# Kernel tuning notes

Hardware: AMD Instinct MI355X
Metric: run time of the kernel (lower is better)

Reference implementation:

```python
import jax, jax.numpy as jnp
import numpy as np

FP4_MAX = 6.0
FP8_MAX = 448.0  # float8_e4m3fn max
BLOCK = 16
# representable |values| of fp4 e2m1 and decision midpoints (ties round up)
FP4_LEVELS = jnp.array([0.0, 0.5, 1.0, 1.5, 2.0, 3.0, 4.0, 6.0], dtype=jnp.float32)
FP4_MIDS = jnp.array([0.25, 0.75, 1.25, 1.75, 2.5, 3.5, 5.0], dtype=jnp.float32)


def _fp4_round(x):
    # round to nearest fp4 e2m1 value (magnitudes clamp at 6)
    a = jnp.abs(x)
    idx = jnp.searchsorted(FP4_MIDS, a, side='right')
    return jnp.sign(x) * FP4_LEVELS[idx]


def nvfp4_quant(x, global_scale):
    # x: [M, K] float32 -> (q_fp4 values [M, K], block scales [M, K//16] fp8-representable)
    M, K = x.shape
    xb = x.reshape(M, K // BLOCK, BLOCK)
    block_amax = jnp.max(jnp.abs(xb), axis=-1)  # [M, K//16]
    scale = jnp.clip(block_amax * (global_scale / FP4_MAX), 0.0, FP8_MAX)
    scale = scale.astype(jnp.float8_e4m3fn).astype(jnp.float32)
    safe = jnp.where(scale == 0.0, 1.0, scale)
    q = _fp4_round(xb * (global_scale / safe)[..., None])
    return q.reshape(M, K), scale


def setup_inputs() -> dict:
    key = jax.random.key(0)
    k_in, k_w, k_b = jax.random.split(key, 3)
    M, K, N = 256, 5120, 13824
    x = jax.random.normal(k_in, (M, K), dtype=jnp.float32)
    # build pre-quantized NVFP4 weight buffers (as the module's load_quantized_weights would)
    w = jax.random.normal(k_w, (N, K), dtype=jnp.float32) * 0.02
    w_gs = (FP8_MAX * FP4_MAX) / jnp.max(jnp.abs(w))  # scalar float32
    w_fp4, w_scale = nvfp4_quant(w, w_gs)
    bias = jax.random.normal(k_b, (N,), dtype=jnp.float32) * 0.01
    return {
        'input': x,
        'weight_fp4': w_fp4,            # [N, K] fp4 values held in f32
        'weight_scale': w_scale,        # [N, K//16] fp8_e4m3-representable f32
        'weight_global_scale': w_gs,    # scalar f32
        'bias': bias,                   # [N]
    }


def reference(input, weight_fp4, weight_scale, weight_global_scale, bias):
    # activations cast to bf16 (as in the torch module), math in f32
    x = input.astype(jnp.bfloat16).astype(jnp.float32)
    M, K = x.shape
    N = weight_fp4.shape[0]
    # per-tensor global scale for activations
    a_gs = (FP8_MAX * FP4_MAX) / jnp.max(jnp.abs(x))
    alpha = 1.0 / (a_gs * weight_global_scale)
    # on-the-fly fp4 quantization of activations
    a_fp4, a_scale = nvfp4_quant(x, a_gs)
    # block-scaled dequant-matmul: out = (a_fp4*s_a) @ (w_fp4*s_w)^T * alpha + bias
    a_u = (a_fp4.reshape(M, K // BLOCK, BLOCK) * a_scale[..., None]).reshape(M, K)
    w_u = (weight_fp4.reshape(N, K // BLOCK, BLOCK) * weight_scale[..., None]).reshape(N, K)
    out = jnp.einsum('mk,nk->mn', a_u, w_u) * alpha + bias[None, :]
    return out
```

## Files before the change

kernel.cpp:

```cpp
#include <hip/hip_runtime.h>

typedef __attribute__((ext_vector_type(8))) __bf16 bf16x8;
typedef __attribute__((ext_vector_type(4))) float floatx4;

#define M_TOT 256
#define K_TOT 5120
#define N_TOT 13824
#define NBLK  320
#define BN    64
#define BK    64
#define KSPLIT 4
#define KCH   1280
#define NSTEP 20

#define GLOAD_LDS16(g, l)                                                     \
  __builtin_amdgcn_global_load_lds(                                           \
      (const __attribute__((address_space(1))) void*)(g),                     \
      (__attribute__((address_space(3))) void*)(l), 16, 0, 0)

static __device__ __forceinline__ float bf16r(float v) { return (float)(__bf16)v; }

static __device__ __forceinline__ float fp4round(float v) {
  float a = fabsf(v), q;
  if      (a < 0.25f) q = 0.0f;
  else if (a < 0.75f) q = 0.5f;
  else if (a < 1.25f) q = 1.0f;
  else if (a < 1.75f) q = 1.5f;
  else if (a < 2.5f)  q = 2.0f;
  else if (a < 3.5f)  q = 3.0f;
  else if (a < 5.0f)  q = 4.0f;
  else                q = 6.0f;
  return copysignf(q, v);
}

static __device__ __forceinline__ float cvt_e4m3(float f) {
  if (f < 0.015625f) return rintf(f * 512.0f) * 0.001953125f;
  int e = (int)(__float_as_uint(f) >> 23) - 127;
  float q = __uint_as_float((unsigned)(e - 3 + 127) << 23);
  return rintf(f / q) * q;
}

__global__ void k_amax(const float* __restrict__ x, unsigned* __restrict__ amax_bits) {
  int i = blockIdx.x * blockDim.x + threadIdx.x;
  float4 v = ((const float4*)x)[i];
  float m = fmaxf(fmaxf(fabsf(bf16r(v.x)), fabsf(bf16r(v.y))),
                  fmaxf(fabsf(bf16r(v.z)), fabsf(bf16r(v.w))));
#pragma unroll
  for (int off = 32; off; off >>= 1) m = fmaxf(m, __shfl_xor(m, off));
  if ((threadIdx.x & 63) == 0) atomicMax(amax_bits, __float_as_uint(m));
}

__global__ void k_aquant(const float* __restrict__ x,
                         const unsigned* __restrict__ amax_bits,
                         __bf16* __restrict__ au) {
  int idx = blockIdx.x * blockDim.x + threadIdx.x;
  int m = idx / NBLK;
  int b = idx - m * NBLK;
  float amax = __uint_as_float(*amax_bits);
  float gs  = 2688.0f / amax;
  float gs6 = gs / 6.0f;
  const float4* xp = (const float4*)(x + m * K_TOT + b * 16);
  float4 v0 = xp[0], v1 = xp[1], v2 = xp[2], v3 = xp[3];
  float xv[16];
  xv[0]=bf16r(v0.x); xv[1]=bf16r(v0.y); xv[2]=bf16r(v0.z); xv[3]=bf16r(v0.w);
  xv[4]=bf16r(v1.x); xv[5]=bf16r(v1.y); xv[6]=bf16r(v1.z); xv[7]=bf16r(v1.w);
  xv[8]=bf16r(v2.x); xv[9]=bf16r(v2.y); xv[10]=bf16r(v2.z); xv[11]=bf16r(v2.w);
  xv[12]=bf16r(v3.x); xv[13]=bf16r(v3.y); xv[14]=bf16r(v3.z); xv[15]=bf16r(v3.w);
  float am = 0.f;
#pragma unroll
  for (int j = 0; j < 16; ++j) am = fmaxf(am, fabsf(xv[j]));
  float s = cvt_e4m3(fminf(am * gs6, 448.0f));
  float g = gs / ((s == 0.f) ? 1.f : s);
  bf16x8 p0, p1;
#pragma unroll
  for (int j = 0; j < 8; ++j) p0[j] = (__bf16)(fp4round(xv[j] * g) * s);
#pragma unroll
  for (int j = 0; j < 8; ++j) p1[j] = (__bf16)(fp4round(xv[8 + j] * g) * s);
  bf16x8* dst = (bf16x8*)(au + (size_t)idx * 16);
  dst[0] = p0; dst[1] = p1;
}

__global__ __launch_bounds__(512, 4) void k_gemm(
    const __bf16* __restrict__ au,
    const float*  __restrict__ w,
    const float*  __restrict__ wsc,
    const unsigned* __restrict__ amax_bits,
    const float*  __restrict__ wgs,
    const float*  __restrict__ bias,
    float* __restrict__ out)
{
  __shared__ __bf16 Ab[2][M_TOT * BK];
  __shared__ __bf16 Bb[2][BN * BK];

  const int tid  = threadIdx.x;
  const int lane = tid & 63;
  const int wv   = tid >> 6;
  const int wm   = wv >> 1;
  const int wn   = wv & 1;

  const int s     = blockIdx.x & (KSPLIT - 1);
  const int n0    = (blockIdx.x >> 2) * BN;
  const int kbase = s * KCH;

  const int arow  = wv * 32 + (lane >> 3);
  const int acolp = 8 * ((lane & 7) ^ (lane >> 3));

  const int brow = tid >> 3;
  const int bcg  = tid & 7;
  const float* wp  = w   + (size_t)(n0 + brow) * K_TOT + kbase + bcg * 8;
  const float* wsp = wsc + (size_t)(n0 + brow) * NBLK + s * (KCH / 16) + (bcg >> 1);
  const int bdst = brow * 128 + ((bcg * 16) ^ ((brow & 7) << 4));

  const int sw    = (lane & 7) << 4;
  const int hi    = lane >> 4;
  const int r15   = lane & 15;

  floatx4 acc[4][2];
#pragma unroll
  for (int fm = 0; fm < 4; ++fm)
#pragma unroll
    for (int fn = 0; fn < 2; ++fn) acc[fm][fn] = (floatx4){0.f, 0.f, 0.f, 0.f};

  float4 bv0, bv1; float bs;

  auto issueA = [&](int t, int buf) {
    const __bf16* src = au + (size_t)arow * K_TOT + kbase + t * BK + acolp;
    char* dst = (char*)(&Ab[buf][0]) + wv * 4096;
#pragma unroll
    for (int i = 0; i < 4; ++i)
      GLOAD_LDS16(src + (size_t)i * 8 * K_TOT, dst + i * 1024);
  };
  auto loadB = [&](int t) {
    const float* p = wp + t * BK;
    bv0 = *(const float4*)p;
    bv1 = *(const float4*)(p + 4);
    bs  = wsp[t * 4];
  };
  auto writeB = [&](int buf) {
    float vv[8] = {bv0.x, bv0.y, bv0.z, bv0.w, bv1.x, bv1.y, bv1.z, bv1.w};
    bf16x8 pk;
#pragma unroll
    for (int j = 0; j < 8; ++j) pk[j] = (__bf16)(vv[j] * bs);
    *(bf16x8*)((char*)(&Bb[buf][0]) + bdst) = pk;
  };
  auto compute = [&](int buf) {
    char* pA = (char*)(&Ab[buf][0]);
    char* pB = (char*)(&Bb[buf][0]);
#pragma unroll
    for (int ss = 0; ss < 2; ++ss) {
      const int cb = ss * 64 + hi * 16;
      bf16x8 af[4], bfr[2];
#pragma unroll
      for (int fm = 0; fm < 4; ++fm)
        af[fm] = *(const bf16x8*)(pA + (wm * 64 + fm * 16 + r15) * 128 + (cb ^ sw));
#pragma unroll
      for (int fn = 0; fn < 2; ++fn)
        bfr[fn] = *(const bf16x8*)(pB + (wn * 32 + fn * 16 + r15) * 128 + (cb ^ sw));
#pragma unroll
      for (int fm = 0; fm < 4; ++fm)
#pragma unroll
        for (int fn = 0; fn < 2; ++fn)
          acc[fm][fn] = __builtin_amdgcn_mfma_f32_16x16x32_bf16(af[fm], bfr[fn], acc[fm][fn], 0, 0, 0);
    }
  };

  int buf = 0;
  issueA(0, 0);
  loadB(0);
  writeB(0);
  __syncthreads();
#pragma unroll 1
  for (int t = 0; t < NSTEP; ++t) {
    if (t + 1 < NSTEP) { issueA(t + 1, buf ^ 1); loadB(t + 1); }
    compute(buf);
    if (t + 1 < NSTEP) writeB(buf ^ 1);
    __syncthreads();
    buf ^= 1;
  }

  float amax = __uint_as_float(*amax_bits);
  float a_gs = 2688.0f / amax;
  float alpha = 1.0f / (a_gs * wgs[0]);
#pragma unroll
  for (int fm = 0; fm < 4; ++fm) {
#pragma unroll
    for (int fn = 0; fn < 2; ++fn) {
      int mrow = wm * 64 + fm * 16 + hi * 4;
      int ncol = n0 + wn * 32 + fn * 16 + r15;
      float bb = (s == 0) ? bias[ncol] : 0.0f;
#pragma unroll
      for (int j = 0; j < 4; ++j)
        atomicAdd(&out[(size_t)(mrow + j) * N_TOT + ncol],
                  acc[fm][fn][j] * alpha + bb);
    }
  }
}

extern "C" void kernel_launch(void* const* d_in, const int* in_sizes, int n_in,
                              void* d_out, int out_size, void* d_ws, size_t ws_size,
                              hipStream_t stream) {
  const float* x    = (const float*)d_in[0];
  const float* wq   = (const float*)d_in[1];
  const float* wsc  = (const float*)d_in[2];
  const float* wgs  = (const float*)d_in[3];
  const float* bias = (const float*)d_in[4];
  float* out = (float*)d_out;

  unsigned* amax = (unsigned*)d_ws;
  __bf16* au = (__bf16*)((char*)d_ws + 256);

  hipMemsetAsync(d_ws, 0, 4, stream);
  hipMemsetAsync(d_out, 0, (size_t)M_TOT * N_TOT * sizeof(float), stream);
  k_amax<<<dim3(M_TOT * K_TOT / 4 / 256), dim3(256), 0, stream>>>(x, amax);
  k_aquant<<<dim3(M_TOT * NBLK / 256), dim3(256), 0, stream>>>(x, amax, au);
  k_gemm<<<dim3((N_TOT / BN) * KSPLIT), dim3(512), 0, stream>>>(au, wq, wsc, amax, wgs, bias, out);
}
```

Measured before the change: 209.6 us.

## Halve GEMM K-tile to 32 with new LDS swizzle and custom zero kernel

Shrinks the K step of the split-K GEMM from 64 to 32, which halves the shared-memory footprint per buffer. It also rewrites the A/B load mappings and the XOR swizzle for the 64-byte rows, and computes with a single MFMA sub-step per tile. The intent is to fit more workgroups per CU to hide memory latency. The cost is twice as many loop iterations and barriers, with less work between them. The output memset is also replaced by a dedicated float4 zeroing kernel.

Result: slower. 245.9 us (+17.3%).

```diff
diff --git a/kernel.cpp b/kernel.cpp
--- a/kernel.cpp
+++ b/kernel.cpp
@@ -1,6 +1,7 @@
 #include <hip/hip_runtime.h>
 
 typedef __attribute__((ext_vector_type(8))) __bf16 bf16x8;
+typedef __attribute__((ext_vector_type(4))) __bf16 bf16x4;
 typedef __attribute__((ext_vector_type(4))) float floatx4;
 
 #define M_TOT 256
@@ -8,10 +9,10 @@
 #define N_TOT 13824
 #define NBLK  320
 #define BN    64
-#define BK    64
+#define BK    32
 #define KSPLIT 4
 #define KCH   1280
-#define NSTEP 20
+#define NSTEP 40
 
 #define GLOAD_LDS16(g, l)                                                     \
   __builtin_amdgcn_global_load_lds(                                           \
@@ -38,6 +39,12 @@
   int e = (int)(__float_as_uint(f) >> 23) - 127;
   float q = __uint_as_float((unsigned)(e - 3 + 127) << 23);
   return rintf(f / q) * q;
+}
+
+__global__ void k_zero(float4* __restrict__ out4) {
+  int idx = blockIdx.x * blockDim.x + threadIdx.x;
+#pragma unroll
+  for (int i = 0; i < 4; ++i) out4[idx + i * 221184] = (float4){0.f, 0.f, 0.f, 0.f};
 }
 
 __global__ void k_amax(const float* __restrict__ x, unsigned* __restrict__ amax_bits) {
@@ -102,18 +109,19 @@
   const int n0    = (blockIdx.x >> 2) * BN;
   const int kbase = s * KCH;
 
-  const int arow  = wv * 32 + (lane >> 3);
-  const int acolp = 8 * ((lane & 7) ^ (lane >> 3));
+  const int arow  = wv * 32 + (lane >> 2);
+  const int acolp = 8 * ((lane & 3) ^ ((lane >> 2) & 3));
 
   const int brow = tid >> 3;
   const int bcg  = tid & 7;
-  const float* wp  = w   + (size_t)(n0 + brow) * K_TOT + kbase + bcg * 8;
-  const float* wsp = wsc + (size_t)(n0 + brow) * NBLK + s * (KCH / 16) + (bcg >> 1);
-  const int bdst = brow * 128 + ((bcg * 16) ^ ((brow & 7) << 4));
-
-  const int sw    = (lane & 7) << 4;
-  const int hi    = lane >> 4;
-  const int r15   = lane & 15;
+  const float* wp  = w   + (size_t)(n0 + brow) * K_TOT + kbase + bcg * 4;
+  const float* wsp = wsc + (size_t)(n0 + brow) * NBLK + s * (KCH / 16);
+  const int bsci = bcg >> 2;
+  const int bdst = brow * 64 + (((bcg >> 1) ^ (brow & 3)) << 4) + (bcg & 1) * 8;
+
+  const int hi  = lane >> 4;
+  const int r15 = lane & 15;
+  const int sw3 = r15 & 3;
 
   floatx4 acc[4][2];
 #pragma unroll
@@ -121,47 +129,44 @@
 #pragma unroll
     for (int fn = 0; fn < 2; ++fn) acc[fm][fn] = (floatx4){0.f, 0.f, 0.f, 0.f};
 
-  float4 bv0, bv1; float bs;
+  float4 bv; float bs;
 
   auto issueA = [&](int t, int buf) {
     const __bf16* src = au + (size_t)arow * K_TOT + kbase + t * BK + acolp;
-    char* dst = (char*)(&Ab[buf][0]) + wv * 4096;
-#pragma unroll
-    for (int i = 0; i < 4; ++i)
-      GLOAD_LDS16(src + (size_t)i * 8 * K_TOT, dst + i * 1024);
+    char* dst = (char*)(&Ab[buf][0]) + wv * 2048;
+#pragma unroll
+    for (int i = 0; i < 2; ++i)
+      GLOAD_LDS16(src + (size_t)i * 16 * K_TOT, dst + i * 1024);
   };
   auto loadB = [&](int t) {
-    const float* p = wp + t * BK;
-    bv0 = *(const float4*)p;
-    bv1 = *(const float4*)(p + 4);
-    bs  = wsp[t * 4];
+    bv = *(const float4*)(wp + t * BK);
+    bs = wsp[t * 2 + bsci];
   };
   auto writeB = [&](int buf) {
-    float vv[8] = {bv0.x, bv0.y, bv0.z, bv0.w, bv1.x, bv1.y, bv1.z, bv1.w};
-    bf16x8 pk;
-#pragma unroll
-    for (int j = 0; j < 8; ++j) pk[j] = (__bf16)(vv[j] * bs);
-    *(bf16x8*)((char*)(&Bb[buf][0]) + bdst) = pk;
+    bf16x4 pk;
+    pk[0] = (__bf16)(bv.x * bs); pk[1] = (__bf16)(bv.y * bs);
+    pk[2] = (__bf16)(bv.z * bs); pk[3] = (__bf16)(bv.w * bs);
+    *(bf16x4*)((char*)(&Bb[buf][0]) + bdst) = pk;
   };
   auto compute = [&](int buf) {
     char* pA = (char*)(&Ab[buf][0]);
     char* pB = (char*)(&Bb[buf][0]);
-#pragma unroll
-    for (int ss = 0; ss < 2; ++ss) {
-      const int cb = ss * 64 + hi * 16;
-      bf16x8 af[4], bfr[2];
-#pragma unroll
-      for (int fm = 0; fm < 4; ++fm)
-        af[fm] = *(const bf16x8*)(pA + (wm * 64 + fm * 16 + r15) * 128 + (cb ^ sw));
+    bf16x8 af[4], bfr[2];
+#pragma unroll
+    for (int fm = 0; fm < 4; ++fm) {
+      const int row = wm * 64 + fm * 16 + r15;
+      af[fm] = *(const bf16x8*)(pA + row * 64 + ((hi ^ sw3) << 4));
+    }
+#pragma unroll
+    for (int fn = 0; fn < 2; ++fn) {
+      const int row = wn * 32 + fn * 16 + r15;
+      bfr[fn] = *(const bf16x8*)(pB + row * 64 + ((hi ^ sw3) << 4));
+    }
+#pragma unroll
+    for (int fm = 0; fm < 4; ++fm)
 #pragma unroll
       for (int fn = 0; fn < 2; ++fn)
-        bfr[fn] = *(const bf16x8*)(pB + (wn * 32 + fn * 16 + r15) * 128 + (cb ^ sw));
-#pragma unroll
-      for (int fm = 0; fm < 4; ++fm)
-#pragma unroll
-        for (int fn = 0; fn < 2; ++fn)
-          acc[fm][fn] = __builtin_amdgcn_mfma_f32_16x16x32_bf16(af[fm], bfr[fn], acc[fm][fn], 0, 0, 0);
-    }
+        acc[fm][fn] = __builtin_amdgcn_mfma_f32_16x16x32_bf16(af[fm], bfr[fn], acc[fm][fn], 0, 0, 0);
   };
 
   int buf = 0;
@@ -210,7 +215,7 @@
   __bf16* au = (__bf16*)((char*)d_ws + 256);
 
   hipMemsetAsync(d_ws, 0, 4, stream);
-  hipMemsetAsync(d_out, 0, (size_t)M_TOT * N_TOT * sizeof(float), stream);
+  k_zero<<<dim3(864), dim3(256), 0, stream>>>((float4*)out);
   k_amax<<<dim3(M_TOT * K_TOT / 4 / 256), dim3(256), 0, stream>>>(x, amax);
   k_aquant<<<dim3(M_TOT * NBLK / 256), dim3(256), 0, stream>>>(x, amax, au);
   k_gemm<<<dim3((N_TOT / BN) * KSPLIT), dim3(512), 0, stream>>>(au, wq, wsc, amax, wgs, bias, out);
```

## Pack weights into 4-bit nibbles before GEMM and fuse output zeroing

Applied to the files above, without the earlier changes.

A new pre-pass kernel reads the f32 FP4-valued weight matrix once and encodes each element as a 4-bit sign+index nibble, eight per 32-bit word. The GEMM then loads one word per eight weights and decodes them into bf16 with bit manipulation before writing to LDS. This cuts the weight bytes the GEMM streams by a factor of eight. The output memset is folded into the amax kernel to save a launch. The pre-pass still reads the full f32 weights on every call, so total memory traffic does not drop, and the expected benefit depends on the GEMM having been stalled on its weight loads.

Measured after the change: 223.7 us. 6.7% more time.

```diff
diff --git a/kernel.cpp b/kernel.cpp
--- a/kernel.cpp
+++ b/kernel.cpp
@@ -12,6 +12,7 @@
 #define KSPLIT 4
 #define KCH   1280
 #define NSTEP 20
+#define KPACK (K_TOT/8)
 
 #define GLOAD_LDS16(g, l)                                                     \
   __builtin_amdgcn_global_load_lds(                                           \
@@ -40,9 +41,29 @@
   return rintf(f / q) * q;
 }
 
-__global__ void k_amax(const float* __restrict__ x, unsigned* __restrict__ amax_bits) {
+__global__ void k_wpack(const float* __restrict__ w, unsigned* __restrict__ wp) {
   int i = blockIdx.x * blockDim.x + threadIdx.x;
-  float4 v = ((const float4*)x)[i];
+  const float4* p = (const float4*)w + 2 * (size_t)i;
+  float4 a = p[0], b = p[1];
+  float v[8] = {a.x, a.y, a.z, a.w, b.x, b.y, b.z, b.w};
+  unsigned pk = 0;
+#pragma unroll
+  for (int j = 0; j < 8; ++j) {
+    unsigned bits = __float_as_uint(v[j]);
+    unsigned t = (bits >> 22) & 0x1FFu;
+    unsigned idx = (t >= 0xFCu) ? (t - 0xFBu - (t >= 0xFEu)) : 0u;
+    unsigned nib = idx | ((bits >> 28) & 8u);
+    pk |= nib << (4 * j);
+  }
+  wp[i] = pk;
+}
+
+__global__ void k_prep(const float* __restrict__ x, unsigned* __restrict__ amax_bits,
+                       float4* __restrict__ out4) {
+  int idx = blockIdx.x * blockDim.x + threadIdx.x;
+#pragma unroll 1
+  for (int j = idx; j < 884736; j += 327680) out4[j] = (float4){0.f, 0.f, 0.f, 0.f};
+  float4 v = ((const float4*)x)[idx];
   float m = fmaxf(fmaxf(fabsf(bf16r(v.x)), fabsf(bf16r(v.y))),
                   fmaxf(fabsf(bf16r(v.z)), fabsf(bf16r(v.w))));
 #pragma unroll
@@ -82,7 +103,7 @@
 
 __global__ __launch_bounds__(512, 4) void k_gemm(
     const __bf16* __restrict__ au,
-    const float*  __restrict__ w,
+    const unsigned* __restrict__ wp,
     const float*  __restrict__ wsc,
     const unsigned* __restrict__ amax_bits,
     const float*  __restrict__ wgs,
@@ -107,8 +128,8 @@
 
   const int brow = tid >> 3;
   const int bcg  = tid & 7;
-  const float* wp  = w   + (size_t)(n0 + brow) * K_TOT + kbase + bcg * 8;
-  const float* wsp = wsc + (size_t)(n0 + brow) * NBLK + s * (KCH / 16) + (bcg >> 1);
+  const unsigned* wpp = wp + (size_t)(n0 + brow) * KPACK + (kbase >> 3) + bcg;
+  const float*    wsp = wsc + (size_t)(n0 + brow) * NBLK + s * (KCH / 16) + (bcg >> 1);
   const int bdst = brow * 128 + ((bcg * 16) ^ ((brow & 7) << 4));
 
   const int sw    = (lane & 7) << 4;
@@ -121,7 +142,7 @@
 #pragma unroll
     for (int fn = 0; fn < 2; ++fn) acc[fm][fn] = (floatx4){0.f, 0.f, 0.f, 0.f};
 
-  float4 bv0, bv1; float bs;
+  unsigned bpk; float bs;
 
   auto issueA = [&](int t, int buf) {
     const __bf16* src = au + (size_t)arow * K_TOT + kbase + t * BK + acolp;
@@ -131,17 +152,22 @@
       GLOAD_LDS16(src + (size_t)i * 8 * K_TOT, dst + i * 1024);
   };
   auto loadB = [&](int t) {
-    const float* p = wp + t * BK;
-    bv0 = *(const float4*)p;
-    bv1 = *(const float4*)(p + 4);
+    bpk = wpp[t * 8];
     bs  = wsp[t * 4];
   };
   auto writeB = [&](int buf) {
-    float vv[8] = {bv0.x, bv0.y, bv0.z, bv0.w, bv1.x, bv1.y, bv1.z, bv1.w};
-    bf16x8 pk;
-#pragma unroll
-    for (int j = 0; j < 8; ++j) pk[j] = (__bf16)(vv[j] * bs);
-    *(bf16x8*)((char*)(&Bb[buf][0]) + bdst) = pk;
+    bf16x8 pkv;
+#pragma unroll
+    for (int j = 0; j < 8; ++j) {
+      unsigned idx = (bpk >> (4 * j)) & 7u;
+      unsigned sg  = (bpk >> (4 * j + 3)) & 1u;
+      unsigned mb  = (idx == 0) ? 0u
+                   : (idx == 1) ? 0x3F000000u
+                                : 0x3F800000u + ((idx - 2u) << 22);
+      float m = __uint_as_float(mb | (sg << 31));
+      pkv[j] = (__bf16)(m * bs);
+    }
+    *(bf16x8*)((char*)(&Bb[buf][0]) + bdst) = pkv;
   };
   auto compute = [&](int buf) {
     char* pA = (char*)(&Ab[buf][0]);
@@ -208,10 +234,11 @@
 
   unsigned* amax = (unsigned*)d_ws;
   __bf16* au = (__bf16*)((char*)d_ws + 256);
+  unsigned* wpk = (unsigned*)((char*)d_ws + (4u << 20));
 
   hipMemsetAsync(d_ws, 0, 4, stream);
-  hipMemsetAsync(d_out, 0, (size_t)M_TOT * N_TOT * sizeof(float), stream);
-  k_amax<<<dim3(M_TOT * K_TOT / 4 / 256), dim3(256), 0, stream>>>(x, amax);
+  k_wpack<<<dim3(N_TOT * KPACK / 256), dim3(256), 0, stream>>>(wq, wpk);
+  k_prep<<<dim3(1280), dim3(256), 0, stream>>>(x, amax, (float4*)out);
   k_aquant<<<dim3(M_TOT * NBLK / 256), dim3(256), 0, stream>>>(x, amax, au);
-  k_gemm<<<dim3((N_TOT / BN) * KSPLIT), dim3(512), 0, stream>>>(au, wq, wsc, amax, wgs, bias, out);
-}
+  k_gemm<<<dim3((N_TOT / BN) * KSPLIT), dim3(512), 0, stream>>>(au, wpk, wsc, amax, wgs, bias, out);
+}
```

## Pre-dequantize weights to swizzled bf16 tiles and DMA both operands to LDS

Applied to the files above, without the earlier changes.

Adds a k_wdeq kernel that multiplies the fp4 weights by their block scales and writes bf16 in a per-tile, per-k-step swizzled layout. It also makes the activation quant kernel write A in a matching tiled layout. The GEMM then loads both A and B with direct global-to-LDS loads, with no register staging or conversion. Output zeroing moves from a memset into the amax kernel. The cost is a full extra pass over the f32 weights and a bf16 workspace write on every call.

Result: slower. 237.9 us (+13.5%).

```diff
diff --git a/kernel.cpp b/kernel.cpp
--- a/kernel.cpp
+++ b/kernel.cpp
@@ -12,6 +12,8 @@
 #define KSPLIT 4
 #define KCH   1280
 #define NSTEP 20
+#define KSTEPS 80
+#define NTILES 216
 
 #define GLOAD_LDS16(g, l)                                                     \
   __builtin_amdgcn_global_load_lds(                                           \
@@ -40,9 +42,33 @@
   return rintf(f / q) * q;
 }
 
-__global__ void k_amax(const float* __restrict__ x, unsigned* __restrict__ amax_bits) {
-  int i = blockIdx.x * blockDim.x + threadIdx.x;
-  float4 v = ((const float4*)x)[i];
+__global__ void k_wdeq(const float* __restrict__ w, const float* __restrict__ wsc,
+                       __bf16* __restrict__ wt) {
+  int c = blockIdx.x * blockDim.x + threadIdx.x;
+  int chsw = c & 7;
+  int row  = (c >> 3) & 63;
+  int g    = c >> 9;
+  int t    = g % KSTEPS;
+  int nt   = g / KSTEPS;
+  int lch  = chsw ^ (row & 7);
+  int n    = nt * 64 + row;
+  const float* p = w + (size_t)n * K_TOT + t * 64 + lch * 8;
+  float sc = wsc[(size_t)n * NBLK + t * 4 + (lch >> 1)];
+  float4 a = *(const float4*)p, b = *(const float4*)(p + 4);
+  bf16x8 o;
+  o[0] = (__bf16)(a.x * sc); o[1] = (__bf16)(a.y * sc);
+  o[2] = (__bf16)(a.z * sc); o[3] = (__bf16)(a.w * sc);
+  o[4] = (__bf16)(b.x * sc); o[5] = (__bf16)(b.y * sc);
+  o[6] = (__bf16)(b.z * sc); o[7] = (__bf16)(b.w * sc);
+  *(bf16x8*)(wt + (size_t)c * 8) = o;
+}
+
+__global__ void k_prep(const float* __restrict__ x, unsigned* __restrict__ amax_bits,
+                       float4* __restrict__ out4) {
+  int idx = blockIdx.x * blockDim.x + threadIdx.x;
+#pragma unroll 1
+  for (int j = idx; j < 884736; j += 327680) out4[j] = (float4){0.f, 0.f, 0.f, 0.f};
+  float4 v = ((const float4*)x)[idx];
   float m = fmaxf(fmaxf(fabsf(bf16r(v.x)), fabsf(bf16r(v.y))),
                   fmaxf(fabsf(bf16r(v.z)), fabsf(bf16r(v.w))));
 #pragma unroll
@@ -76,14 +102,15 @@
   for (int j = 0; j < 8; ++j) p0[j] = (__bf16)(fp4round(xv[j] * g) * s);
 #pragma unroll
   for (int j = 0; j < 8; ++j) p1[j] = (__bf16)(fp4round(xv[8 + j] * g) * s);
-  bf16x8* dst = (bf16x8*)(au + (size_t)idx * 16);
-  dst[0] = p0; dst[1] = p1;
+  int t = b >> 2, pr = b & 3;
+  __bf16* base = au + (size_t)(t * 256 + m) * 64;
+  *(bf16x8*)(base + (((2 * pr)     ^ (m & 7)) * 8)) = p0;
+  *(bf16x8*)(base + (((2 * pr + 1) ^ (m & 7)) * 8)) = p1;
 }
 
 __global__ __launch_bounds__(512, 4) void k_gemm(
     const __bf16* __restrict__ au,
-    const float*  __restrict__ w,
-    const float*  __restrict__ wsc,
+    const __bf16* __restrict__ wt,
     const unsigned* __restrict__ amax_bits,
     const float*  __restrict__ wgs,
     const float*  __restrict__ bias,
@@ -98,22 +125,17 @@
   const int wm   = wv >> 1;
   const int wn   = wv & 1;
 
-  const int s     = blockIdx.x & (KSPLIT - 1);
-  const int n0    = (blockIdx.x >> 2) * BN;
-  const int kbase = s * KCH;
-
-  const int arow  = wv * 32 + (lane >> 3);
-  const int acolp = 8 * ((lane & 7) ^ (lane >> 3));
-
-  const int brow = tid >> 3;
-  const int bcg  = tid & 7;
-  const float* wp  = w   + (size_t)(n0 + brow) * K_TOT + kbase + bcg * 8;
-  const float* wsp = wsc + (size_t)(n0 + brow) * NBLK + s * (KCH / 16) + (bcg >> 1);
-  const int bdst = brow * 128 + ((bcg * 16) ^ ((brow & 7) << 4));
-
-  const int sw    = (lane & 7) << 4;
-  const int hi    = lane >> 4;
-  const int r15   = lane & 15;
+  const int s    = blockIdx.x & (KSPLIT - 1);
+  const int nt   = blockIdx.x >> 2;
+  const int n0   = nt * BN;
+  const int s20  = s * NSTEP;
+
+  const int sw  = (lane & 7) << 4;
+  const int hi  = lane >> 4;
+  const int r15 = lane & 15;
+
+  const __bf16* asrc = au + (size_t)s20 * 16384 + (wv * 32) * 64 + lane * 8;
+  const __bf16* bsrc = wt + ((size_t)nt * KSTEPS + s20) * 4096 + wv * 512 + lane * 8;
 
   floatx4 acc[4][2];
 #pragma unroll
@@ -121,27 +143,13 @@
 #pragma unroll
     for (int fn = 0; fn < 2; ++fn) acc[fm][fn] = (floatx4){0.f, 0.f, 0.f, 0.f};
 
-  float4 bv0, bv1; float bs;
-
-  auto issueA = [&](int t, int buf) {
-    const __bf16* src = au + (size_t)arow * K_TOT + kbase + t * BK + acolp;
-    char* dst = (char*)(&Ab[buf][0]) + wv * 4096;
+  auto issueAB = [&](int t, int buf) {
+    const __bf16* a = asrc + (size_t)t * 16384;
+    char* dA = (char*)(&Ab[buf][0]) + wv * 4096;
 #pragma unroll
     for (int i = 0; i < 4; ++i)
-      GLOAD_LDS16(src + (size_t)i * 8 * K_TOT, dst + i * 1024);
-  };
-  auto loadB = [&](int t) {
-    const float* p = wp + t * BK;
-    bv0 = *(const float4*)p;
-    bv1 = *(const float4*)(p + 4);
-    bs  = wsp[t * 4];
-  };
-  auto writeB = [&](int buf) {
-    float vv[8] = {bv0.x, bv0.y, bv0.z, bv0.w, bv1.x, bv1.y, bv1.z, bv1.w};
-    bf16x8 pk;
-#pragma unroll
-    for (int j = 0; j < 8; ++j) pk[j] = (__bf16)(vv[j] * bs);
-    *(bf16x8*)((char*)(&Bb[buf][0]) + bdst) = pk;
+      GLOAD_LDS16(a + i * 512, dA + i * 1024);
+    GLOAD_LDS16(bsrc + (size_t)t * 4096, (char*)(&Bb[buf][0]) + wv * 1024);
   };
   auto compute = [&](int buf) {
     char* pA = (char*)(&Ab[buf][0]);
@@ -165,15 +173,12 @@
   };
 
   int buf = 0;
-  issueA(0, 0);
-  loadB(0);
-  writeB(0);
+  issueAB(0, 0);
   __syncthreads();
 #pragma unroll 1
   for (int t = 0; t < NSTEP; ++t) {
-    if (t + 1 < NSTEP) { issueA(t + 1, buf ^ 1); loadB(t + 1); }
+    if (t + 1 < NSTEP) issueAB(t + 1, buf ^ 1);
     compute(buf);
-    if (t + 1 < NSTEP) writeB(buf ^ 1);
     __syncthreads();
     buf ^= 1;
   }
@@ -208,10 +213,11 @@
 
   unsigned* amax = (unsigned*)d_ws;
   __bf16* au = (__bf16*)((char*)d_ws + 256);
+  __bf16* wt = (__bf16*)((char*)d_ws + (4ull << 20));
 
   hipMemsetAsync(d_ws, 0, 4, stream);
-  hipMemsetAsync(d_out, 0, (size_t)M_TOT * N_TOT * sizeof(float), stream);
-  k_amax<<<dim3(M_TOT * K_TOT / 4 / 256), dim3(256), 0, stream>>>(x, amax);
+  k_wdeq<<<dim3(N_TOT * K_TOT / 8 / 256), dim3(256), 0, stream>>>(wq, wsc, wt);
+  k_prep<<<dim3(1280), dim3(256), 0, stream>>>(x, amax, (float4*)out);
   k_aquant<<<dim3(M_TOT * NBLK / 256), dim3(256), 0, stream>>>(x, amax, au);
-  k_gemm<<<dim3((N_TOT / BN) * KSPLIT), dim3(512), 0, stream>>>(au, wq, wsc, amax, wgs, bias, out);
-}
+  k_gemm<<<dim3(NTILES * KSPLIT), dim3(512), 0, stream>>>(au, wt, amax, wgs, bias, out);
+}
```
